# Kernel tuning notes

Hardware: AMD Instinct MI355X
Metric: run time of the kernel (lower is better)

Reference implementation:

```python
import jax, jax.numpy as jnp
import numpy as np

N_NODES = 100000
N_EDGES = 1600000
IN_CH = 128
HID = 128
OUT_DIM = 1
N_LAYERS = 3
N_GRAPHS = 512


def setup_inputs() -> dict:
    key = jax.random.key(0)
    ks = jax.random.split(key, 12)
    x = jax.random.normal(ks[0], (N_NODES, IN_CH), dtype=jnp.float32)
    edge_index = jax.random.randint(ks[1], (2, N_EDGES), 0, N_NODES, dtype=jnp.int64)
    batch = jnp.sort(jax.random.randint(ks[2], (N_NODES,), 0, N_GRAPHS, dtype=jnp.int64))
    # GCNConv weights (glorot) and biases; layer 0: in->hid, rest hid->hid (all 128x128 here)
    def glorot(k, fan_in, fan_out):
        lim = jnp.sqrt(6.0 / (fan_in + fan_out)).astype(jnp.float32)
        return jax.random.uniform(k, (fan_in, fan_out), jnp.float32, -lim, lim)
    Ws = jnp.stack([glorot(ks[3 + i], IN_CH if i == 0 else HID, HID) for i in range(N_LAYERS)])
    bs = jnp.zeros((N_LAYERS, HID), dtype=jnp.float32)
    head_w = glorot(ks[8], HID, OUT_DIM)  # stored as [hid, out] == head_weight.T
    head_b = jnp.zeros((OUT_DIM,), dtype=jnp.float32)
    return {"x": x, "edge_index": edge_index, "batch": batch,
            "Ws": Ws, "bs": bs, "head_w": head_w, "head_b": head_b}


def _gcn_norm(edge_index, n_nodes):
    # PyG gcn_norm: add self-loops, deg over dst, norm = d^-1/2[src]*d^-1/2[dst]
    loops = jnp.arange(n_nodes, dtype=edge_index.dtype)
    src = jnp.concatenate([edge_index[0], loops])
    dst = jnp.concatenate([edge_index[1], loops])
    deg = jax.ops.segment_sum(jnp.ones_like(dst, dtype=jnp.float32), dst, num_segments=n_nodes)
    dinv = jnp.where(deg > 0, jax.lax.rsqrt(deg), 0.0)
    norm = dinv[src] * dinv[dst]
    return src, dst, norm


def reference(x, edge_index, batch, Ws, bs, head_w, head_b):
    n = x.shape[0]
    src, dst, norm = _gcn_norm(edge_index, n)
    h = x.astype(jnp.float32)
    for i in range(N_LAYERS):
        t = h @ Ws[i]                                   # [N, hid]
        msg = t[src] * norm[:, None]                    # gather + scale [E+N, hid]
        h = jax.ops.segment_sum(msg, dst, num_segments=n) + bs[i]
        h = jax.nn.relu(h)                              # dropout p=0 -> identity
    g = jax.ops.segment_sum(h, batch, num_segments=N_GRAPHS)  # global_add_pool
    out = g @ head_w + head_b                           # [G, 1]
    return out.reshape(-1)                              # squeeze out_dim==1
```

## Files before the change

### kernel.cpp

```cpp
#include <hip/hip_runtime.h>

#define NN 100000
#define NE 1600000
#define CH 128
#define NG 512
#define NL 3
#define BSZ 512
#define NBUK ((NN + BSZ - 1) / BSZ)
#define TILE 4096

typedef short bf8 __attribute__((ext_vector_type(8)));
typedef float f4 __attribute__((ext_vector_type(4)));
typedef unsigned int u32x4 __attribute__((ext_vector_type(4)));
typedef unsigned short u16;
typedef unsigned int u32;

__device__ __forceinline__ long long ld_idx(const void* p, long long i, bool is64) {
    return is64 ? ((const long long*)p)[i] : (long long)((const int*)p)[i];
}
__device__ __forceinline__ u16 f2bf(float f) {
    u32 u = __float_as_uint(f);
    u += 0x7fffu + ((u >> 16) & 1u);
    return (u16)(u >> 16);
}
__device__ __forceinline__ float bflo(u32 v) { return __uint_as_float(v << 16); }
__device__ __forceinline__ float bfhi(u32 v) { return __uint_as_float(v & 0xffff0000u); }

__global__ void k_zero(int* bcnt, int* flags) {
    int i = blockIdx.x * blockDim.x + threadIdx.x;
    if (i < NBUK) bcnt[i] = 0;
    if (i < 2) flags[i] = 0;
}

__global__ void k_detect(const int* __restrict__ ei32, const int* __restrict__ b32, int* flags) {
    int acc_e = 0, acc_b = 0;
    long long stride = (long long)gridDim.x * blockDim.x;
    long long t0 = (long long)blockIdx.x * blockDim.x + threadIdx.x;
    for (long long i = t0; i < NE; i += stride) acc_e |= ei32[2 * i + 1];
    for (long long i = t0; i < NN / 2; i += stride) acc_b |= b32[2 * i + 1];
    if (acc_e) atomicOr(&flags[0], 1);
    if (acc_b) atomicOr(&flags[1], 1);
}


__global__ __launch_bounds__(256) void k_hist(const void* __restrict__ ei,
                                              const int* __restrict__ flags,
                                              int* __restrict__ bcnt) {
    __shared__ int cnt[NBUK];
    int tid = threadIdx.x;
    long long e0 = (long long)blockIdx.x * TILE;
    bool is64 = (flags[0] == 0);
    for (int b = tid; b < NBUK; b += 256) cnt[b] = 0;
    __syncthreads();
#pragma unroll
    for (int k = 0; k < 16; ++k) {
        long long e = e0 + tid + k * 256;
        if (e < NE) {
            int d = (int)ld_idx(ei, NE + e, is64);
            atomicAdd(&cnt[d >> 9], 1);
        }
    }
    __syncthreads();
    for (int b = tid; b < NBUK; b += 256)
        if (cnt[b]) atomicAdd(&bcnt[b], cnt[b]);
}

__global__ __launch_bounds__(256) void k_bscan(const int* __restrict__ bcnt,
                                               int* __restrict__ gbase,
                                               int* __restrict__ gcur,
                                               int* __restrict__ rowptr) {
    __shared__ int ws4[4];
    int t = threadIdx.x;
    int v = (t < NBUK) ? bcnt[t] : 0;
    int x = v;
#pragma unroll
    for (int d = 1; d < 64; d <<= 1) {
        int y = __shfl_up(x, d, 64);
        if ((t & 63) >= d) x += y;
    }
    if ((t & 63) == 63) ws4[t >> 6] = x;
    __syncthreads();
    if (t == 0) {
        int s = 0;
#pragma unroll
        for (int w = 0; w < 4; ++w) { int tmp = ws4[w]; ws4[w] = s; s += tmp; }
    }
    __syncthreads();
    int ex = x - v + ws4[t >> 6];
    if (t < NBUK) { gbase[t] = ex; gcur[t] = ex; }
    if (t == NBUK - 1) gbase[NBUK] = ex + v;
    if (t == 0) rowptr[NN] = NE;
}

__global__ __launch_bounds__(256) void k_bin(const void* __restrict__ ei,
                                             const int* __restrict__ flags,
                                             int* __restrict__ gcur,
                                             u32* __restrict__ bin) {
    __shared__ u32 stag[TILE];
    __shared__ int cnt[NBUK], loff[NBUK], lcur[NBUK], gb_s[NBUK];
    int tid = threadIdx.x;
    long long e0 = (long long)blockIdx.x * TILE;
    bool is64 = (flags[0] == 0);

    u32 rec[16];
    int bk[16];
#pragma unroll
    for (int k = 0; k < 16; ++k) {
        long long e = e0 + tid + k * 256;
        if (e < NE) {
            int s = (int)ld_idx(ei, e, is64);
            int d = (int)ld_idx(ei, NE + e, is64);
            rec[k] = ((u32)s << 9) | (u32)(d & (BSZ - 1));
            bk[k] = d >> 9;
        } else bk[k] = -1;
    }
    for (int b = tid; b < NBUK; b += 256) { cnt[b] = 0; lcur[b] = 0; }
    __syncthreads();
#pragma unroll
    for (int k = 0; k < 16; ++k)
        if (bk[k] >= 0) atomicAdd(&cnt[bk[k]], 1);
    __syncthreads();
    if (tid == 0) {
        int run = 0;
        for (int b = 0; b < NBUK; ++b) { loff[b] = run; run += cnt[b]; }
    }
    __syncthreads();
    if (tid < NBUK && cnt[tid] > 0) gb_s[tid] = atomicAdd(&gcur[tid], cnt[tid]);
    __syncthreads();
#pragma unroll
    for (int k = 0; k < 16; ++k)
        if (bk[k] >= 0) {
            int pos = loff[bk[k]] + atomicAdd(&lcur[bk[k]], 1);
            stag[pos] = rec[k];
        }
    __syncthreads();
    int wv = tid >> 6, lane = tid & 63;
    for (int b = wv; b < NBUK; b += 4) {
        int n = cnt[b];
        int gb = (n > 0) ? gb_s[b] : 0;
        int lo = loff[b];
        for (int j = lane; j < n; j += 64) bin[gb + j] = stag[lo + j];
    }
}

__global__ __launch_bounds__(512) void k_fillc(const u32* __restrict__ bin,
                                               const int* __restrict__ gbase,
                                               int* __restrict__ rowptr,
                                               float* __restrict__ dinv,
                                               u32* __restrict__ csr) {
    __shared__ int cnt[BSZ];
    __shared__ int lcur[BSZ];
    __shared__ int wsum[8];
    int b = blockIdx.x, tid = threadIdx.x;
    int gb = gbase[b], ge = gbase[b + 1];
    cnt[tid] = 0;
    __syncthreads();
    for (int i = gb + tid; i < ge; i += BSZ)
        atomicAdd(&cnt[bin[i] & (BSZ - 1)], 1);
    __syncthreads();
    int v = cnt[tid];
    int x = v;
#pragma unroll
    for (int d = 1; d < 64; d <<= 1) {
        int y = __shfl_up(x, d, 64);
        if ((tid & 63) >= d) x += y;
    }
    if ((tid & 63) == 63) wsum[tid >> 6] = x;
    __syncthreads();
    if (tid == 0) {
        int s = 0;
#pragma unroll
        for (int w = 0; w < 8; ++w) { int tmp = wsum[w]; wsum[w] = s; s += tmp; }
    }
    __syncthreads();
    int off = gb + x - v + wsum[tid >> 6];
    int node = b * BSZ + tid;
    if (node < NN) {
        rowptr[node] = off;
        dinv[node] = rsqrtf((float)v + 1.0f);
    }
    lcur[tid] = off;
    __syncthreads();
    for (int i = gb + tid; i < ge; i += BSZ) {
        u32 rec = bin[i];
        int pos = atomicAdd(&lcur[rec & (BSZ - 1)], 1);
        csr[pos] = rec >> 9;
    }
}

__global__ void k_cvt(const float* __restrict__ x, u16* __restrict__ xb,
                      const float* __restrict__ Ws, u16* __restrict__ Wt) {
    long long i = ((long long)blockIdx.x * blockDim.x + threadIdx.x) * 4;
    const long long NX = (long long)NN * CH;
    if (i < NX) {
        float4 v = *(const float4*)(x + i);
        ushort4 o;
        o.x = f2bf(v.x); o.y = f2bf(v.y); o.z = f2bf(v.z); o.w = f2bf(v.w);
        *(ushort4*)(xb + i) = o;
    } else {
        int j = (int)(i - NX);
        if (j >= NL * CH * CH) return;
        int l = j >> 14, c = (j >> 7) & 127, k = j & 127;
        ushort4 o;
        o.x = f2bf(Ws[(l << 14) + ((k + 0) << 7) + c]);
        o.y = f2bf(Ws[(l << 14) + ((k + 1) << 7) + c]);
        o.z = f2bf(Ws[(l << 14) + ((k + 2) << 7) + c]);
        o.w = f2bf(Ws[(l << 14) + ((k + 3) << 7) + c]);
        *(ushort4*)(Wt + j) = o;
    }
}

__global__ __launch_bounds__(256) void k_mm(const u16* __restrict__ A,
                                            const u16* __restrict__ Wt,
                                            u16* __restrict__ out) {
    int tid = threadIdx.x;
    int lane = tid & 63;
    int wv = tid >> 6;
    int rbase = blockIdx.x * 128 + wv * 32;
    int lm = lane & 15;
    int lk = (lane >> 4) << 3;

    f4 acc[2][8];
#pragma unroll
    for (int m = 0; m < 2; ++m)
#pragma unroll
        for (int n = 0; n < 8; ++n) acc[m][n] = (f4){0.f, 0.f, 0.f, 0.f};

    int r0 = rbase + lm;      if (r0 >= NN) r0 = NN - 1;
    int r1 = rbase + 16 + lm; if (r1 >= NN) r1 = NN - 1;

#pragma unroll
    for (int kk = 0; kk < 4; ++kk) {
        int ko = kk * 32 + lk;
        bf8 a0 = *(const bf8*)(A + (size_t)r0 * CH + ko);
        bf8 a1 = *(const bf8*)(A + (size_t)r1 * CH + ko);
#pragma unroll
        for (int n = 0; n < 8; ++n) {
            bf8 b = *(const bf8*)(Wt + (n * 16 + lm) * CH + ko);
            acc[0][n] = __builtin_amdgcn_mfma_f32_16x16x32_bf16(a0, b, acc[0][n], 0, 0, 0);
            acc[1][n] = __builtin_amdgcn_mfma_f32_16x16x32_bf16(a1, b, acc[1][n], 0, 0, 0);
        }
    }

#pragma unroll
    for (int m = 0; m < 2; ++m) {
        int rb = rbase + m * 16 + (lane >> 4) * 4;
#pragma unroll
        for (int r = 0; r < 4; ++r) {
            int row = rb + r;
            if (row < NN) {
#pragma unroll
                for (int n = 0; n < 8; ++n)
                    out[(size_t)row * CH + n * 16 + lm] = f2bf(acc[m][n][r]);
            }
        }
    }
}

#define ACC8(v, w) \
    acc[0] = fmaf(bflo(v[0]), w, acc[0]); acc[1] = fmaf(bfhi(v[0]), w, acc[1]); \
    acc[2] = fmaf(bflo(v[1]), w, acc[2]); acc[3] = fmaf(bfhi(v[1]), w, acc[3]); \
    acc[4] = fmaf(bflo(v[2]), w, acc[4]); acc[5] = fmaf(bfhi(v[2]), w, acc[5]); \
    acc[6] = fmaf(bflo(v[3]), w, acc[6]); acc[7] = fmaf(bfhi(v[3]), w, acc[7]);

__global__ __launch_bounds__(256) void k_aggr(const u16* __restrict__ t,
                                              const int* __restrict__ rowptr,
                                              const u32* __restrict__ csr,
                                              const float* __restrict__ dinv,
                                              const float* __restrict__ b,
                                              u16* __restrict__ h,
                                              const float* __restrict__ hw,
                                              float* __restrict__ partial) {
    int node = (blockIdx.x << 2) + (threadIdx.x >> 6);
    if (node >= NN) return;
    int lane = threadIdx.x & 63;
    int g = lane >> 4;
    int l16 = lane & 15;
    int c8 = l16 << 3;
    const u32x4* tp = (const u32x4*)t;

    int beg = rowptr[node], end = rowptr[node + 1];
    float dn = dinv[node];
    float acc[8];
#pragma unroll
    for (int k = 0; k < 8; ++k) acc[k] = 0.f;

    for (int base = beg; base < end; base += 64) {
        int srcv = 0;
        float wl = 0.f;
        if (base + lane < end) {
            srcv = (int)csr[base + lane];
            wl = dinv[srcv] * dn;
        }
        int cnt = min(64, end - base);
        for (int j0 = 0; j0 < cnt; j0 += 16) {
            int s0 = __shfl(srcv, j0 + g);
            int s1 = __shfl(srcv, j0 + 4 + g);
            int s2 = __shfl(srcv, j0 + 8 + g);
            int s3 = __shfl(srcv, j0 + 12 + g);
            float w0 = __shfl(wl, j0 + g);
            float w1 = __shfl(wl, j0 + 4 + g);
            float w2 = __shfl(wl, j0 + 8 + g);
            float w3 = __shfl(wl, j0 + 12 + g);
            u32x4 v0 = tp[s0 * 16 + l16];
            u32x4 v1 = tp[s1 * 16 + l16];
            u32x4 v2 = tp[s2 * 16 + l16];
            u32x4 v3 = tp[s3 * 16 + l16];
            ACC8(v0, w0); ACC8(v1, w1); ACC8(v2, w2); ACC8(v3, w3);
        }
    }
#pragma unroll
    for (int k = 0; k < 8; ++k) {
        acc[k] += __shfl_xor(acc[k], 16);
        acc[k] += __shfl_xor(acc[k], 32);
    }
    float sl = dn * dn;
    u32x4 sv = tp[node * 16 + l16];
    float r[8];
    r[0] = fmaf(bflo(sv[0]), sl, acc[0]); r[1] = fmaf(bfhi(sv[0]), sl, acc[1]);
    r[2] = fmaf(bflo(sv[1]), sl, acc[2]); r[3] = fmaf(bfhi(sv[1]), sl, acc[3]);
    r[4] = fmaf(bflo(sv[2]), sl, acc[4]); r[5] = fmaf(bfhi(sv[2]), sl, acc[5]);
    r[6] = fmaf(bflo(sv[3]), sl, acc[6]); r[7] = fmaf(bfhi(sv[3]), sl, acc[7]);
    float4 b0 = *(const float4*)(b + c8);
    float4 b1 = *(const float4*)(b + c8 + 4);
    r[0] = fmaxf(r[0] + b0.x, 0.f); r[1] = fmaxf(r[1] + b0.y, 0.f);
    r[2] = fmaxf(r[2] + b0.z, 0.f); r[3] = fmaxf(r[3] + b0.w, 0.f);
    r[4] = fmaxf(r[4] + b1.x, 0.f); r[5] = fmaxf(r[5] + b1.y, 0.f);
    r[6] = fmaxf(r[6] + b1.z, 0.f); r[7] = fmaxf(r[7] + b1.w, 0.f);

    if (hw) {
        float4 w0 = *(const float4*)(hw + c8);
        float4 w1 = *(const float4*)(hw + c8 + 4);
        float d = r[0] * w0.x + r[1] * w0.y + r[2] * w0.z + r[3] * w0.w
                + r[4] * w1.x + r[5] * w1.y + r[6] * w1.z + r[7] * w1.w;
#pragma unroll
        for (int off = 8; off > 0; off >>= 1) d += __shfl_xor(d, off);
        if (lane == 0) partial[node] = d;
    } else if (g == 0) {
        u32x4 o;
        o[0] = ((u32)f2bf(r[1]) << 16) | (u32)f2bf(r[0]);
        o[1] = ((u32)f2bf(r[3]) << 16) | (u32)f2bf(r[2]);
        o[2] = ((u32)f2bf(r[5]) << 16) | (u32)f2bf(r[4]);
        o[3] = ((u32)f2bf(r[7]) << 16) | (u32)f2bf(r[6]);
        ((u32x4*)h)[node * 16 + l16] = o;
    }
}


__device__ __forceinline__ int lbound(const void* bt, bool is64, int target) {
    int lo = 0, hi = NN;
    while (lo < hi) {
        int mid = (lo + hi) >> 1;
        long long v = ld_idx(bt, mid, is64);
        if (v < (long long)target) lo = mid + 1; else hi = mid;
    }
    return lo;
}

__global__ __launch_bounds__(256) void k_head(const float* __restrict__ partial,
                                              const void* __restrict__ batch,
                                              const int* __restrict__ flags,
                                              const float* __restrict__ hb,
                                              float* __restrict__ out) {
    int g = blockIdx.x * 4 + (threadIdx.x >> 6);
    if (g >= NG) return;
    int lane = threadIdx.x & 63;
    bool is64 = (flags[1] == 0);
    int lo = lbound(batch, is64, g);
    int hi = lbound(batch, is64, g + 1);
    float s = 0.f;
    for (int i = lo + lane; i < hi; i += 64) s += partial[i];
#pragma unroll
    for (int off = 32; off > 0; off >>= 1) s += __shfl_down(s, off);
    if (lane == 0) out[g] = s + hb[0];
}

extern "C" void kernel_launch(void* const* d_in, const int* in_sizes, int n_in,
                              void* d_out, int out_size, void* d_ws, size_t ws_size,
                              hipStream_t stream) {
    const float* x  = (const float*)d_in[0];
    const void*  ei = d_in[1];
    const void*  bt = d_in[2];
    const float* Ws = (const float*)d_in[3];
    const float* bs = (const float*)d_in[4];
    const float* hw = (const float*)d_in[5];
    const float* hb = (const float*)d_in[6];
    float* out = (float*)d_out;

    char* ws = (char*)d_ws;
    size_t p = 0;
    auto alloc = [&](size_t bytes) { size_t r = p; p += (bytes + 255) & ~(size_t)255; return r; };
    size_t o_flags  = alloc(256);
    size_t o_dinv   = alloc((size_t)NN * 4);
    size_t o_rowptr = alloc((size_t)(NN + 1) * 4);
    size_t o_bcnt   = alloc((size_t)NBUK * 4);
    size_t o_gbase  = alloc((size_t)(NBUK + 1) * 4);
    size_t o_gcur   = alloc((size_t)NBUK * 4);
    size_t o_part   = alloc((size_t)NN * 4);
    size_t o_bin    = alloc((size_t)NE * 4);
    size_t o_csr    = alloc((size_t)NE * 4);
    size_t o_xb     = alloc((size_t)NN * CH * 2);
    size_t o_tb     = alloc((size_t)NN * CH * 2);
    size_t o_hb     = alloc((size_t)NN * CH * 2);
    size_t o_wt     = alloc((size_t)NL * CH * CH * 2);
    (void)ws_size;

    int*   flags  = (int*)(ws + o_flags);
    float* dinv   = (float*)(ws + o_dinv);
    int*   rowptr = (int*)(ws + o_rowptr);
    int*   bcnt   = (int*)(ws + o_bcnt);
    int*   gbase  = (int*)(ws + o_gbase);
    int*   gcur   = (int*)(ws + o_gcur);
    float* part   = (float*)(ws + o_part);
    u32*   bin    = (u32*)(ws + o_bin);
    u32*   csr    = (u32*)(ws + o_csr);
    u16*   xb     = (u16*)(ws + o_xb);
    u16*   tb     = (u16*)(ws + o_tb);
    u16*   hbuf   = (u16*)(ws + o_hb);
    u16*   Wt     = (u16*)(ws + o_wt);

    k_zero<<<1, 256, 0, stream>>>(bcnt, flags);
    k_detect<<<256, 256, 0, stream>>>((const int*)ei, (const int*)bt, flags);
    k_hist<<<(NE + TILE - 1) / TILE, 256, 0, stream>>>(ei, flags, bcnt);
    k_bscan<<<1, 256, 0, stream>>>(bcnt, gbase, gcur, rowptr);
    k_bin<<<(NE + TILE - 1) / TILE, 256, 0, stream>>>(ei, flags, gcur, bin);
    k_fillc<<<NBUK, BSZ, 0, stream>>>(bin, gbase, rowptr, dinv, csr);

    long long ncv = (long long)NN * CH / 4 + NL * CH * CH / 4;
    k_cvt<<<(int)((ncv + 255) / 256), 256, 0, stream>>>(x, xb, Ws, Wt);

    const u16* hin = xb;
    for (int l = 0; l < NL; ++l) {
        bool last = (l == NL - 1);
        k_mm<<<(NN + 127) / 128, 256, 0, stream>>>(hin, Wt + (size_t)l * CH * CH, tb);
        k_aggr<<<(NN + 3) / 4, 256, 0, stream>>>(tb, rowptr, csr, dinv,
                                                 bs + (size_t)l * CH, hbuf,
                                                 last ? hw : nullptr, part);
        hin = hbuf;
    }

    k_head<<<(NG + 3) / 4, 256, 0, stream>>>(part, bt, flags, hb, out);
}
```

Measured before the change: 376.9 us.

## Map 16 lanes per node in GCN aggregation and shrink index-width detection scan

The aggregation kernel now gives each destination node a 16-lane group instead of a full 64-lane wave, so a wave serves four nodes. Each lane walks the node's CSR edges sequentially, unrolled by four. This removes the shuffle broadcasts of source indices and weights and the cross-group reduction at the end. The destination dinv factor is applied once after accumulation rather than per edge. Separately, the index-width detection kernel now scans only the first 2^18 edges instead of all of them, which cuts its memory traffic but makes the int32/int64 check a heuristic.

After: 373.2 us. No clear change (-1.0%).

```diff
diff --git a/kernel.cpp b/kernel.cpp
--- a/kernel.cpp
+++ b/kernel.cpp
@@ -36,7 +36,7 @@
     int acc_e = 0, acc_b = 0;
     long long stride = (long long)gridDim.x * blockDim.x;
     long long t0 = (long long)blockIdx.x * blockDim.x + threadIdx.x;
-    for (long long i = t0; i < NE; i += stride) acc_e |= ei32[2 * i + 1];
+    for (long long i = t0; i < (1 << 18); i += stride) acc_e |= ei32[2 * i + 1];
     for (long long i = t0; i < NN / 2; i += stride) acc_b |= b32[2 * i + 1];
     if (acc_e) atomicOr(&flags[0], 1);
     if (acc_b) atomicOr(&flags[1], 1);
@@ -257,7 +257,7 @@
     }
 }
 
-#define ACC8(v, w) \
+#define ACC8W(v, w) \
     acc[0] = fmaf(bflo(v[0]), w, acc[0]); acc[1] = fmaf(bfhi(v[0]), w, acc[1]); \
     acc[2] = fmaf(bflo(v[1]), w, acc[2]); acc[3] = fmaf(bfhi(v[1]), w, acc[3]); \
     acc[4] = fmaf(bflo(v[2]), w, acc[4]); acc[5] = fmaf(bfhi(v[2]), w, acc[5]); \
@@ -271,11 +271,9 @@
                                               u16* __restrict__ h,
                                               const float* __restrict__ hw,
                                               float* __restrict__ partial) {
-    int node = (blockIdx.x << 2) + (threadIdx.x >> 6);
+    int node = blockIdx.x * 16 + (threadIdx.x >> 4);
     if (node >= NN) return;
-    int lane = threadIdx.x & 63;
-    int g = lane >> 4;
-    int l16 = lane & 15;
+    int l16 = threadIdx.x & 15;
     int c8 = l16 << 3;
     const u32x4* tp = (const u32x4*)t;
 
@@ -285,48 +283,36 @@
 #pragma unroll
     for (int k = 0; k < 8; ++k) acc[k] = 0.f;
 
-    for (int base = beg; base < end; base += 64) {
-        int srcv = 0;
-        float wl = 0.f;
-        if (base + lane < end) {
-            srcv = (int)csr[base + lane];
-            wl = dinv[srcv] * dn;
-        }
-        int cnt = min(64, end - base);
-        for (int j0 = 0; j0 < cnt; j0 += 16) {
-            int s0 = __shfl(srcv, j0 + g);
-            int s1 = __shfl(srcv, j0 + 4 + g);
-            int s2 = __shfl(srcv, j0 + 8 + g);
-            int s3 = __shfl(srcv, j0 + 12 + g);
-            float w0 = __shfl(wl, j0 + g);
-            float w1 = __shfl(wl, j0 + 4 + g);
-            float w2 = __shfl(wl, j0 + 8 + g);
-            float w3 = __shfl(wl, j0 + 12 + g);
-            u32x4 v0 = tp[s0 * 16 + l16];
-            u32x4 v1 = tp[s1 * 16 + l16];
-            u32x4 v2 = tp[s2 * 16 + l16];
-            u32x4 v3 = tp[s3 * 16 + l16];
-            ACC8(v0, w0); ACC8(v1, w1); ACC8(v2, w2); ACC8(v3, w3);
-        }
-    }
-#pragma unroll
-    for (int k = 0; k < 8; ++k) {
-        acc[k] += __shfl_xor(acc[k], 16);
-        acc[k] += __shfl_xor(acc[k], 32);
-    }
-    float sl = dn * dn;
+    int j = beg;
+    for (; j + 4 <= end; j += 4) {
+        int s0 = (int)csr[j], s1 = (int)csr[j + 1];
+        int s2 = (int)csr[j + 2], s3 = (int)csr[j + 3];
+        float w0 = dinv[s0], w1 = dinv[s1], w2 = dinv[s2], w3 = dinv[s3];
+        u32x4 v0 = tp[s0 * 16 + l16];
+        u32x4 v1 = tp[s1 * 16 + l16];
+        u32x4 v2 = tp[s2 * 16 + l16];
+        u32x4 v3 = tp[s3 * 16 + l16];
+        ACC8W(v0, w0); ACC8W(v1, w1); ACC8W(v2, w2); ACC8W(v3, w3);
+    }
+    for (; j < end; ++j) {
+        int s = (int)csr[j];
+        float w = dinv[s];
+        u32x4 v = tp[s * 16 + l16];
+        ACC8W(v, w);
+    }
+
     u32x4 sv = tp[node * 16 + l16];
-    float r[8];
-    r[0] = fmaf(bflo(sv[0]), sl, acc[0]); r[1] = fmaf(bfhi(sv[0]), sl, acc[1]);
-    r[2] = fmaf(bflo(sv[1]), sl, acc[2]); r[3] = fmaf(bfhi(sv[1]), sl, acc[3]);
-    r[4] = fmaf(bflo(sv[2]), sl, acc[4]); r[5] = fmaf(bfhi(sv[2]), sl, acc[5]);
-    r[6] = fmaf(bflo(sv[3]), sl, acc[6]); r[7] = fmaf(bfhi(sv[3]), sl, acc[7]);
     float4 b0 = *(const float4*)(b + c8);
     float4 b1 = *(const float4*)(b + c8 + 4);
-    r[0] = fmaxf(r[0] + b0.x, 0.f); r[1] = fmaxf(r[1] + b0.y, 0.f);
-    r[2] = fmaxf(r[2] + b0.z, 0.f); r[3] = fmaxf(r[3] + b0.w, 0.f);
-    r[4] = fmaxf(r[4] + b1.x, 0.f); r[5] = fmaxf(r[5] + b1.y, 0.f);
-    r[6] = fmaxf(r[6] + b1.z, 0.f); r[7] = fmaxf(r[7] + b1.w, 0.f);
+    float r[8];
+    r[0] = fmaxf(fmaf(fmaf(bflo(sv[0]), dn, acc[0]), dn, b0.x), 0.f);
+    r[1] = fmaxf(fmaf(fmaf(bfhi(sv[0]), dn, acc[1]), dn, b0.y), 0.f);
+    r[2] = fmaxf(fmaf(fmaf(bflo(sv[1]), dn, acc[2]), dn, b0.z), 0.f);
+    r[3] = fmaxf(fmaf(fmaf(bfhi(sv[1]), dn, acc[3]), dn, b0.w), 0.f);
+    r[4] = fmaxf(fmaf(fmaf(bflo(sv[2]), dn, acc[4]), dn, b1.x), 0.f);
+    r[5] = fmaxf(fmaf(fmaf(bfhi(sv[2]), dn, acc[5]), dn, b1.y), 0.f);
+    r[6] = fmaxf(fmaf(fmaf(bflo(sv[3]), dn, acc[6]), dn, b1.z), 0.f);
+    r[7] = fmaxf(fmaf(fmaf(bfhi(sv[3]), dn, acc[7]), dn, b1.w), 0.f);
 
     if (hw) {
         float4 w0 = *(const float4*)(hw + c8);
@@ -335,8 +321,8 @@
                 + r[4] * w1.x + r[5] * w1.y + r[6] * w1.z + r[7] * w1.w;
 #pragma unroll
         for (int off = 8; off > 0; off >>= 1) d += __shfl_xor(d, off);
-        if (lane == 0) partial[node] = d;
-    } else if (g == 0) {
+        if (l16 == 0) partial[node] = d;
+    } else {
         u32x4 o;
         o[0] = ((u32)f2bf(r[1]) << 16) | (u32)f2bf(r[0]);
         o[1] = ((u32)f2bf(r[3]) << 16) | (u32)f2bf(r[2]);
@@ -433,9 +419,9 @@
     for (int l = 0; l < NL; ++l) {
         bool last = (l == NL - 1);
         k_mm<<<(NN + 127) / 128, 256, 0, stream>>>(hin, Wt + (size_t)l * CH * CH, tb);
-        k_aggr<<<(NN + 3) / 4, 256, 0, stream>>>(tb, rowptr, csr, dinv,
-                                                 bs + (size_t)l * CH, hbuf,
-                                                 last ? hw : nullptr, part);
+        k_aggr<<<(NN + 15) / 16, 256, 0, stream>>>(tb, rowptr, csr, dinv,
+                                                   bs + (size_t)l * CH, hbuf,
+                                                   last ? hw : nullptr, part);
         hin = hbuf;
     }
 
```
